# Kernel optimization log

Measured on AMD Instinct MI355X. Metric: run time of the kernel, lower is better.

The kernel has to match this reference:

```python
import jax, jax.numpy as jnp
import numpy as np

B, N, D_IN, D_HID, D_OUT = 8, 4096, 64, 128, 64
NEG = -1e16


def setup_inputs() -> dict:
    key = jax.random.key(0)
    k1, k2, k3, k4, k5, k6 = jax.random.split(key, 6)
    flow_x = jax.random.normal(k1, (B, N, D_IN), dtype=jnp.float32)
    adj = (jax.random.uniform(k2, (N, N)) < 0.02).astype(jnp.float32)
    graph = adj.at[jnp.arange(N), jnp.arange(N)].set(1.0)
    W1 = jax.random.normal(k3, (D_HID, D_IN), dtype=jnp.float32)
    b1 = jax.random.normal(k4, (D_HID,), dtype=jnp.float32)
    W2 = jax.random.normal(k5, (D_OUT, D_HID), dtype=jnp.float32)
    b2 = jax.random.normal(k6, (D_OUT,), dtype=jnp.float32)
    return {"flow_x": flow_x, "graph": graph, "W1": W1, "b1": b1, "W2": W2, "b2": b2}


def _gat_layer(x, graph, W, b):
    # h = Linear(x) with weight [out,in], no bias
    h = jnp.einsum('bnd,hd->bnh', x, W)
    # dense masked attention scores [B,N,N]
    s = jnp.einsum('bnh,bmh->bnm', h, h) * graph[None]
    s = jnp.where(s == 0.0, NEG, s)  # masked_fill of zeros (torch semantics)
    a = jax.nn.softmax(s, axis=2)
    return jnp.einsum('bnm,bmh->bnh', a, h) + b


def reference(flow_x, graph, W1, b1, W2, b2):
    out = _gat_layer(flow_x, graph, W1, b1)
    out = jax.nn.relu(out)
    out = _gat_layer(out, graph, W2, b2)
    return out[:, :, None, :]  # unsqueeze(2) -> [B, N, 1, D_OUT]
```

## Files before the change

kernel.cpp:

```cpp
#include <hip/hip_runtime.h>
#include <hip/hip_bf16.h>
#include <cmath>

#define B_   8
#define N_   4096
#define DIN1 64
#define DHID 128
#define DOUT2 64
#define MAXDEG 256

__global__ __launch_bounds__(256) void k_build_csr(
    const float* __restrict__ graph, int* __restrict__ cnt, int* __restrict__ idx)
{
    const int n = blockIdx.x;
    __shared__ int lcnt;
    if (threadIdx.x == 0) lcnt = 0;
    __syncthreads();
    const float4* row4 = (const float4*)(graph + (size_t)n * N_);
    int* myidx = idx + (size_t)n * MAXDEG;
    for (int m4 = threadIdx.x; m4 < N_ / 4; m4 += 256) {
        float4 g = row4[m4];
        if (g.x != 0.0f) { int p = atomicAdd(&lcnt, 1); if (p < MAXDEG) myidx[p] = 4 * m4; }
        if (g.y != 0.0f) { int p = atomicAdd(&lcnt, 1); if (p < MAXDEG) myidx[p] = 4 * m4 + 1; }
        if (g.z != 0.0f) { int p = atomicAdd(&lcnt, 1); if (p < MAXDEG) myidx[p] = 4 * m4 + 2; }
        if (g.w != 0.0f) { int p = atomicAdd(&lcnt, 1); if (p < MAXDEG) myidx[p] = 4 * m4 + 3; }
    }
    __syncthreads();
    if (threadIdx.x == 0) cnt[n] = (lcnt < MAXDEG) ? lcnt : MAXDEG;
}

template <int DIN, int DOUT>
__global__ __launch_bounds__(256) void k_linear(
    const float* __restrict__ x, const float* __restrict__ W,
    float* __restrict__ out)
{
    constexpr int CG = DOUT / 4;
    constexpr int RG = 256 / CG;
    constexpr int TR = 32 / RG;

    __shared__ float sWt[DIN][DOUT + 4];

    const int t = threadIdx.x;
    const float4* W4 = (const float4*)W;
    for (int i = t; i < DOUT * (DIN / 4); i += 256) {
        int kk = i / (DIN / 4);
        int d4 = i % (DIN / 4);
        float4 w = W4[i];
        sWt[4 * d4 + 0][kk] = w.x;
        sWt[4 * d4 + 1][kk] = w.y;
        sWt[4 * d4 + 2][kk] = w.z;
        sWt[4 * d4 + 3][kk] = w.w;
    }
    __syncthreads();

    const int rg = t / CG;
    const int c  = t % CG;
    const int base = blockIdx.x * 32;
    const float4* x4 = (const float4*)x;

    float acc[TR][4];
#pragma unroll
    for (int i = 0; i < TR; ++i)
#pragma unroll
        for (int j = 0; j < 4; ++j) acc[i][j] = 0.0f;

    for (int d4 = 0; d4 < DIN / 4; ++d4) {
        float4 xf[TR];
#pragma unroll
        for (int i = 0; i < TR; ++i)
            xf[i] = x4[(size_t)(base + rg * TR + i) * (DIN / 4) + d4];
        float4 wf[4];
#pragma unroll
        for (int dd = 0; dd < 4; ++dd)
            wf[dd] = *(const float4*)&sWt[4 * d4 + dd][4 * c];
#pragma unroll
        for (int i = 0; i < TR; ++i) {
            acc[i][0] += xf[i].x * wf[0].x + xf[i].y * wf[1].x + xf[i].z * wf[2].x + xf[i].w * wf[3].x;
            acc[i][1] += xf[i].x * wf[0].y + xf[i].y * wf[1].y + xf[i].z * wf[2].y + xf[i].w * wf[3].y;
            acc[i][2] += xf[i].x * wf[0].z + xf[i].y * wf[1].z + xf[i].z * wf[2].z + xf[i].w * wf[3].z;
            acc[i][3] += xf[i].x * wf[0].w + xf[i].y * wf[1].w + xf[i].z * wf[2].w + xf[i].w * wf[3].w;
        }
    }

#pragma unroll
    for (int i = 0; i < TR; ++i) {
        float4 o = {acc[i][0], acc[i][1], acc[i][2], acc[i][3]};
        ((float4*)out)[(size_t)(base + rg * TR + i) * CG + c] = o;
    }
}

template <int D, bool RELU>
__global__ __launch_bounds__(256) void k_attn(
    const float* __restrict__ h, const int* __restrict__ cnt,
    const int* __restrict__ idx, const float* __restrict__ bias,
    float* __restrict__ out)
{
    constexpr int V  = D / 4;
    constexpr int NF = V / 8;

    const int bid  = blockIdx.x;
    const int b    = bid & 7;
    const int wave = threadIdx.x >> 6;
    const int lane = threadIdx.x & 63;
    const int n    = (bid >> 3) * 4 + wave;
    const int grp  = lane >> 3;
    const int gl   = lane & 7;

    __shared__ int s_nbr[4][MAXDEG];

    const int k = cnt[n];
    for (int j = lane; j < k; j += 64)
        s_nbr[wave][j] = idx[(size_t)n * MAXDEG + j];

    const float4* __restrict__ hb4 = (const float4*)(h + (size_t)b * N_ * D);
    float4 qf[NF];
#pragma unroll
    for (int i = 0; i < NF; ++i) qf[i] = hb4[(size_t)n * V + gl + 8 * i];

    float m = -INFINITY, s = 0.0f;
    float4 acc[NF];
#pragma unroll
    for (int i = 0; i < NF; ++i) acc[i] = {0.0f, 0.0f, 0.0f, 0.0f};

    float4 r[NF];
    int j = grp;
    if (j < k) {
        const float4* hm = hb4 + (size_t)s_nbr[wave][j] * V;
#pragma unroll
        for (int i = 0; i < NF; ++i) r[i] = hm[gl + 8 * i];
    }
    while (j < k) {
        float4 cur[NF];
#pragma unroll
        for (int i = 0; i < NF; ++i) cur[i] = r[i];
        const int jn = j + 8;
        if (jn < k) {
            const float4* hm = hb4 + (size_t)s_nbr[wave][jn] * V;
#pragma unroll
            for (int i = 0; i < NF; ++i) r[i] = hm[gl + 8 * i];
        }
        float p = 0.0f;
#pragma unroll
        for (int i = 0; i < NF; ++i)
            p += qf[i].x * cur[i].x + qf[i].y * cur[i].y
               + qf[i].z * cur[i].z + qf[i].w * cur[i].w;
        p += __shfl_xor(p, 4, 64);
        p += __shfl_xor(p, 2, 64);
        p += __shfl_xor(p, 1, 64);
        if (p != 0.0f) {
            if (p > m + 60.0f) {
                const float f = __expf(m - p);
                s = s * f + 1.0f;
#pragma unroll
                for (int i = 0; i < NF; ++i) {
                    acc[i].x = acc[i].x * f + cur[i].x;
                    acc[i].y = acc[i].y * f + cur[i].y;
                    acc[i].z = acc[i].z * f + cur[i].z;
                    acc[i].w = acc[i].w * f + cur[i].w;
                }
                m = p;
            } else {
                const float e = __expf(p - m);
                s += e;
#pragma unroll
                for (int i = 0; i < NF; ++i) {
                    acc[i].x += e * cur[i].x;
                    acc[i].y += e * cur[i].y;
                    acc[i].z += e * cur[i].z;
                    acc[i].w += e * cur[i].w;
                }
            }
        }
        j = jn;
    }

#pragma unroll
    for (int mask = 8; mask <= 32; mask <<= 1) {
        const float m2 = __shfl_xor(m, mask, 64);
        const float s2 = __shfl_xor(s, mask, 64);
        float4 a2[NF];
#pragma unroll
        for (int i = 0; i < NF; ++i) {
            a2[i].x = __shfl_xor(acc[i].x, mask, 64);
            a2[i].y = __shfl_xor(acc[i].y, mask, 64);
            a2[i].z = __shfl_xor(acc[i].z, mask, 64);
            a2[i].w = __shfl_xor(acc[i].w, mask, 64);
        }
        const float mm = fmaxf(m, m2);
        const float f1 = (m  == mm) ? 1.0f : __expf(m  - mm);
        const float f2 = (m2 == mm) ? 1.0f : __expf(m2 - mm);
        s = s * f1 + s2 * f2;
#pragma unroll
        for (int i = 0; i < NF; ++i) {
            acc[i].x = acc[i].x * f1 + a2[i].x * f2;
            acc[i].y = acc[i].y * f1 + a2[i].y * f2;
            acc[i].z = acc[i].z * f1 + a2[i].z * f2;
            acc[i].w = acc[i].w * f1 + a2[i].w * f2;
        }
        m = mm;
    }

    if (s > 0.0f) {
        if (grp == 0) {
            const float4* bias4 = (const float4*)bias;
            const float inv = 1.0f / s;
#pragma unroll
            for (int i = 0; i < NF; ++i) {
                const float4 bi = bias4[gl + 8 * i];
                float4 o;
                o.x = acc[i].x * inv + bi.x;
                o.y = acc[i].y * inv + bi.y;
                o.z = acc[i].z * inv + bi.z;
                o.w = acc[i].w * inv + bi.w;
                if (RELU) {
                    o.x = fmaxf(o.x, 0.0f); o.y = fmaxf(o.y, 0.0f);
                    o.z = fmaxf(o.z, 0.0f); o.w = fmaxf(o.w, 0.0f);
                }
                ((float4*)out)[((size_t)b * N_ + n) * V + gl + 8 * i] = o;
            }
        }
    } else {
        constexpr int RS = 64 / V;
        const int sl = lane % V;
        const int rs = lane / V;
        float4 a = {0.0f, 0.0f, 0.0f, 0.0f};
        for (int row = rs; row < N_; row += RS) {
            float4 v = hb4[(size_t)row * V + sl];
            a.x += v.x; a.y += v.y; a.z += v.z; a.w += v.w;
        }
#pragma unroll
        for (int mask = V; mask < 64; mask <<= 1) {
            a.x += __shfl_xor(a.x, mask, 64);
            a.y += __shfl_xor(a.y, mask, 64);
            a.z += __shfl_xor(a.z, mask, 64);
            a.w += __shfl_xor(a.w, mask, 64);
        }
        if (lane < V) {
            constexpr float invN = 1.0f / (float)N_;
            const float4 bi = ((const float4*)bias)[sl];
            float4 o;
            o.x = a.x * invN + bi.x;
            o.y = a.y * invN + bi.y;
            o.z = a.z * invN + bi.z;
            o.w = a.w * invN + bi.w;
            if (RELU) {
                o.x = fmaxf(o.x, 0.0f); o.y = fmaxf(o.y, 0.0f);
                o.z = fmaxf(o.z, 0.0f); o.w = fmaxf(o.w, 0.0f);
            }
            ((float4*)out)[((size_t)b * N_ + n) * V + sl] = o;
        }
    }
}

extern "C" void kernel_launch(void* const* d_in, const int* in_sizes, int n_in,
                              void* d_out, int out_size, void* d_ws, size_t ws_size,
                              hipStream_t stream) {
    (void)in_sizes; (void)n_in; (void)out_size; (void)ws_size;

    const float* flow_x = (const float*)d_in[0];
    const float* graph  = (const float*)d_in[1];
    const float* W1     = (const float*)d_in[2];
    const float* b1     = (const float*)d_in[3];
    const float* W2     = (const float*)d_in[4];
    const float* b2     = (const float*)d_in[5];
    float* out = (float*)d_out;

    char* p = (char*)d_ws;
    auto carve = [&](size_t bytes) -> void* {
        void* r = (void*)p;
        p += (bytes + 255) & ~(size_t)255;
        return r;
    };
    int*   nbr_cnt = (int*)carve((size_t)N_ * sizeof(int));
    int*   nbr_idx = (int*)carve((size_t)N_ * MAXDEG * sizeof(int));
    float* h1      = (float*)carve((size_t)B_ * N_ * DHID * sizeof(float));
    float* x2      = (float*)carve((size_t)B_ * N_ * DHID * sizeof(float));
    float* h2      = (float*)carve((size_t)B_ * N_ * DOUT2 * sizeof(float));

    k_build_csr<<<N_, 256, 0, stream>>>(graph, nbr_cnt, nbr_idx);

    k_linear<DIN1, DHID><<<(B_ * N_) / 32, 256, 0, stream>>>(flow_x, W1, h1);

    k_attn<DHID, true><<<N_ * B_ / 4, 256, 0, stream>>>(h1, nbr_cnt, nbr_idx, b1, x2);

    k_linear<DHID, DOUT2><<<(B_ * N_) / 32, 256, 0, stream>>>(x2, W2, h2);

    k_attn<DOUT2, false><<<N_ * B_ / 4, 256, 0, stream>>>(h2, nbr_cnt, nbr_idx, b2, out);
}
```

Before: 270.4 us.

## Use 16-lane neighbor groups, triple-buffer row loads, branchless online softmax

Each neighbor row is now handled by 16 lanes instead of 8, so a wave processes 4 neighbors at a time with fewer registers per lane and one extra shuffle in the dot product. The single prefetch buffer becomes a rotating three-buffer pipeline that keeps two neighbor-row loads in flight. The divergent rescale branch in the online softmax is replaced by a branchless max/exp update. The cost is more loop iterations per row, because each wave covers fewer neighbors per step, and two exp evaluations on every update.

New measurement: 297.3 us. 9.9% more time.

```diff
diff --git a/kernel.cpp b/kernel.cpp
--- a/kernel.cpp
+++ b/kernel.cpp
@@ -96,15 +96,15 @@
     float* __restrict__ out)
 {
     constexpr int V  = D / 4;
-    constexpr int NF = V / 8;
+    constexpr int NF = V / 16;
 
     const int bid  = blockIdx.x;
     const int b    = bid & 7;
     const int wave = threadIdx.x >> 6;
     const int lane = threadIdx.x & 63;
     const int n    = (bid >> 3) * 4 + wave;
-    const int grp  = lane >> 3;
-    const int gl   = lane & 7;
+    const int grp  = lane >> 4;
+    const int gl   = lane & 15;
 
     __shared__ int s_nbr[4][MAXDEG];
 
@@ -115,67 +115,68 @@
     const float4* __restrict__ hb4 = (const float4*)(h + (size_t)b * N_ * D);
     float4 qf[NF];
 #pragma unroll
-    for (int i = 0; i < NF; ++i) qf[i] = hb4[(size_t)n * V + gl + 8 * i];
+    for (int i = 0; i < NF; ++i) qf[i] = hb4[(size_t)n * V + gl + 16 * i];
 
     float m = -INFINITY, s = 0.0f;
     float4 acc[NF];
 #pragma unroll
     for (int i = 0; i < NF; ++i) acc[i] = {0.0f, 0.0f, 0.0f, 0.0f};
 
-    float4 r[NF];
-    int j = grp;
-    if (j < k) {
-        const float4* hm = hb4 + (size_t)s_nbr[wave][j] * V;
-#pragma unroll
-        for (int i = 0; i < NF; ++i) r[i] = hm[gl + 8 * i];
-    }
-    while (j < k) {
-        float4 cur[NF];
-#pragma unroll
-        for (int i = 0; i < NF; ++i) cur[i] = r[i];
-        const int jn = j + 8;
-        if (jn < k) {
-            const float4* hm = hb4 + (size_t)s_nbr[wave][jn] * V;
-#pragma unroll
-            for (int i = 0; i < NF; ++i) r[i] = hm[gl + 8 * i];
-        }
+    auto process = [&](const float4 (&cur)[NF]) {
         float p = 0.0f;
 #pragma unroll
         for (int i = 0; i < NF; ++i)
             p += qf[i].x * cur[i].x + qf[i].y * cur[i].y
                + qf[i].z * cur[i].z + qf[i].w * cur[i].w;
+        p += __shfl_xor(p, 8, 64);
         p += __shfl_xor(p, 4, 64);
         p += __shfl_xor(p, 2, 64);
         p += __shfl_xor(p, 1, 64);
-        if (p != 0.0f) {
-            if (p > m + 60.0f) {
-                const float f = __expf(m - p);
-                s = s * f + 1.0f;
-#pragma unroll
-                for (int i = 0; i < NF; ++i) {
-                    acc[i].x = acc[i].x * f + cur[i].x;
-                    acc[i].y = acc[i].y * f + cur[i].y;
-                    acc[i].z = acc[i].z * f + cur[i].z;
-                    acc[i].w = acc[i].w * f + cur[i].w;
-                }
-                m = p;
-            } else {
-                const float e = __expf(p - m);
-                s += e;
-#pragma unroll
-                for (int i = 0; i < NF; ++i) {
-                    acc[i].x += e * cur[i].x;
-                    acc[i].y += e * cur[i].y;
-                    acc[i].z += e * cur[i].z;
-                    acc[i].w += e * cur[i].w;
-                }
-            }
-        }
-        j = jn;
-    }
-
-#pragma unroll
-    for (int mask = 8; mask <= 32; mask <<= 1) {
+        const bool valid = (p != 0.0f);
+        const float pm   = valid ? p : m;
+        const float newm = fmaxf(m, pm);
+        const float f = (m == newm) ? 1.0f : __expf(m - newm);
+        const float e = valid ? __expf(p - newm) : 0.0f;
+        s = s * f + e;
+#pragma unroll
+        for (int i = 0; i < NF; ++i) {
+            acc[i].x = acc[i].x * f + e * cur[i].x;
+            acc[i].y = acc[i].y * f + e * cur[i].y;
+            acc[i].z = acc[i].z * f + e * cur[i].z;
+            acc[i].w = acc[i].w * f + e * cur[i].w;
+        }
+        m = newm;
+    };
+
+    auto loadrow = [&](float4 (&r)[NF], int j) {
+        const float4* hm = hb4 + (size_t)s_nbr[wave][j] * V;
+#pragma unroll
+        for (int i = 0; i < NF; ++i) r[i] = hm[gl + 16 * i];
+    };
+
+    float4 r0[NF], r1[NF], r2[NF];
+    {
+        int j = grp;
+        if (j     < k) loadrow(r0, j);
+        if (j + 4 < k) loadrow(r1, j + 4);
+        while (true) {
+            if (j >= k) break;
+            if (j + 8 < k) loadrow(r2, j + 8);
+            process(r0);
+            j += 4;
+            if (j >= k) break;
+            if (j + 8 < k) loadrow(r0, j + 8);
+            process(r1);
+            j += 4;
+            if (j >= k) break;
+            if (j + 8 < k) loadrow(r1, j + 8);
+            process(r2);
+            j += 4;
+        }
+    }
+
+#pragma unroll
+    for (int mask = 16; mask <= 32; mask <<= 1) {
         const float m2 = __shfl_xor(m, mask, 64);
         const float s2 = __shfl_xor(s, mask, 64);
         float4 a2[NF];
@@ -206,7 +207,7 @@
             const float inv = 1.0f / s;
 #pragma unroll
             for (int i = 0; i < NF; ++i) {
-                const float4 bi = bias4[gl + 8 * i];
+                const float4 bi = bias4[gl + 16 * i];
                 float4 o;
                 o.x = acc[i].x * inv + bi.x;
                 o.y = acc[i].y * inv + bi.y;
@@ -216,7 +217,7 @@
                     o.x = fmaxf(o.x, 0.0f); o.y = fmaxf(o.y, 0.0f);
                     o.z = fmaxf(o.z, 0.0f); o.w = fmaxf(o.w, 0.0f);
                 }
-                ((float4*)out)[((size_t)b * N_ + n) * V + gl + 8 * i] = o;
+                ((float4*)out)[((size_t)b * N_ + n) * V + gl + 16 * i] = o;
             }
         }
     } else {
```

## Regroup attention lanes to 16 per row and triple-buffer neighbor row loads

Applied to the files above, without the earlier changes.

The sparse attention kernel now assigns 16 lanes per neighbor row, so each wave handles 4 rows at a time instead of 8. It keeps three register buffers, prefetching two rows ahead to hide gather latency. Neighbor indices are turned into byte offsets in shared memory ahead of time, padded with zero offsets so prefetches past the end are safe. The running max is seeded with the node's self-score, so the online-softmax rescale branch should rarely run; this also replaces the old +60 tolerance with an exact max test. In exchange, register pressure rises and fewer rows are processed at once per wave.

New measurement: 270.1 us. About the same (-0.1%).

```diff
diff --git a/kernel.cpp b/kernel.cpp
--- a/kernel.cpp
+++ b/kernel.cpp
@@ -96,59 +96,67 @@
     float* __restrict__ out)
 {
     constexpr int V  = D / 4;
-    constexpr int NF = V / 8;
+    constexpr int NF = V / 16;
+    constexpr int RB = D * 4;
 
     const int bid  = blockIdx.x;
     const int b    = bid & 7;
     const int wave = threadIdx.x >> 6;
     const int lane = threadIdx.x & 63;
     const int n    = (bid >> 3) * 4 + wave;
-    const int grp  = lane >> 3;
-    const int gl   = lane & 7;
-
-    __shared__ int s_nbr[4][MAXDEG];
+    const int grp  = lane >> 4;
+    const int gl   = lane & 15;
+
+    __shared__ int s_off[4][MAXDEG + 12];
 
     const int k = cnt[n];
-    for (int j = lane; j < k; j += 64)
-        s_nbr[wave][j] = idx[(size_t)n * MAXDEG + j];
-
-    const float4* __restrict__ hb4 = (const float4*)(h + (size_t)b * N_ * D);
+    const int* __restrict__ myidx = idx + (size_t)n * MAXDEG;
+    for (int j = lane; j < k; j += 64) s_off[wave][j] = myidx[j] * RB;
+    if (lane < 12) s_off[wave][k + lane] = 0;
+
+    const char* __restrict__ hb = (const char*)h + (size_t)b * N_ * RB;
+    const int lb = gl * 16;
+
     float4 qf[NF];
 #pragma unroll
-    for (int i = 0; i < NF; ++i) qf[i] = hb4[(size_t)n * V + gl + 8 * i];
-
-    float m = -INFINITY, s = 0.0f;
+    for (int i = 0; i < NF; ++i)
+        qf[i] = *(const float4*)(hb + (size_t)n * RB + lb + 256 * i);
+
+    float m;
+    {
+        float p = 0.0f;
+#pragma unroll
+        for (int i = 0; i < NF; ++i)
+            p += qf[i].x * qf[i].x + qf[i].y * qf[i].y
+               + qf[i].z * qf[i].z + qf[i].w * qf[i].w;
+        p += __shfl_xor(p, 8, 64);
+        p += __shfl_xor(p, 4, 64);
+        p += __shfl_xor(p, 2, 64);
+        p += __shfl_xor(p, 1, 64);
+        m = (p != 0.0f) ? p : -INFINITY;
+    }
+    float s = 0.0f;
     float4 acc[NF];
 #pragma unroll
     for (int i = 0; i < NF; ++i) acc[i] = {0.0f, 0.0f, 0.0f, 0.0f};
 
-    float4 r[NF];
-    int j = grp;
-    if (j < k) {
-        const float4* hm = hb4 + (size_t)s_nbr[wave][j] * V;
-#pragma unroll
-        for (int i = 0; i < NF; ++i) r[i] = hm[gl + 8 * i];
-    }
-    while (j < k) {
-        float4 cur[NF];
-#pragma unroll
-        for (int i = 0; i < NF; ++i) cur[i] = r[i];
-        const int jn = j + 8;
-        if (jn < k) {
-            const float4* hm = hb4 + (size_t)s_nbr[wave][jn] * V;
-#pragma unroll
-            for (int i = 0; i < NF; ++i) r[i] = hm[gl + 8 * i];
-        }
+    auto loadrow = [&](float4 (&r)[NF], int j) {
+        const char* hm = hb + s_off[wave][j];
+#pragma unroll
+        for (int i = 0; i < NF; ++i) r[i] = *(const float4*)(hm + lb + 256 * i);
+    };
+    auto process = [&](const float4 (&cur)[NF]) {
         float p = 0.0f;
 #pragma unroll
         for (int i = 0; i < NF; ++i)
             p += qf[i].x * cur[i].x + qf[i].y * cur[i].y
                + qf[i].z * cur[i].z + qf[i].w * cur[i].w;
+        p += __shfl_xor(p, 8, 64);
         p += __shfl_xor(p, 4, 64);
         p += __shfl_xor(p, 2, 64);
         p += __shfl_xor(p, 1, 64);
         if (p != 0.0f) {
-            if (p > m + 60.0f) {
+            if (__builtin_expect(p > m, 0)) {
                 const float f = __expf(m - p);
                 s = s * f + 1.0f;
 #pragma unroll
@@ -171,11 +179,28 @@
                 }
             }
         }
-        j = jn;
-    }
-
-#pragma unroll
-    for (int mask = 8; mask <= 32; mask <<= 1) {
+    };
+
+    {
+        float4 r0[NF], r1[NF], r2[NF];
+        loadrow(r0, grp);
+        loadrow(r1, grp + 4);
+        int j = grp;
+        while (j < k) {
+            loadrow(r2, j + 8);
+            process(r0);
+            j += 4; if (j >= k) break;
+            loadrow(r0, j + 8);
+            process(r1);
+            j += 4; if (j >= k) break;
+            loadrow(r1, j + 8);
+            process(r2);
+            j += 4;
+        }
+    }
+
+#pragma unroll
+    for (int mask = 16; mask <= 32; mask <<= 1) {
         const float m2 = __shfl_xor(m, mask, 64);
         const float s2 = __shfl_xor(s, mask, 64);
         float4 a2[NF];
@@ -206,7 +231,7 @@
             const float inv = 1.0f / s;
 #pragma unroll
             for (int i = 0; i < NF; ++i) {
-                const float4 bi = bias4[gl + 8 * i];
+                const float4 bi = bias4[gl + 16 * i];
                 float4 o;
                 o.x = acc[i].x * inv + bi.x;
                 o.y = acc[i].y * inv + bi.y;
@@ -216,10 +241,11 @@
                     o.x = fmaxf(o.x, 0.0f); o.y = fmaxf(o.y, 0.0f);
                     o.z = fmaxf(o.z, 0.0f); o.w = fmaxf(o.w, 0.0f);
                 }
-                ((float4*)out)[((size_t)b * N_ + n) * V + gl + 8 * i] = o;
+                ((float4*)out)[((size_t)b * N_ + n) * V + gl + 16 * i] = o;
             }
         }
     } else {
+        const float4* hb4 = (const float4*)hb;
         constexpr int RS = 64 / V;
         const int sl = lane % V;
         const int rs = lane / V;
```
